# Kernel optimization log

Hardware: AMD Instinct MI355X
Metric: run time of the kernel (lower is better)

Reference implementation:

```python
import jax, jax.numpy as jnp
import numpy as np

# Dimensions
B = 256        # number of graphs
NPG = 128      # nodes per graph (max_nodes; uniform -> to_dense_batch == reshape)
H = 8          # num_heads
DH = 32        # head_dim
HID = H * DH   # hidden_dim = 256
E = 524288     # n_edges
NGT = 20       # num_gate_types
EF = 8         # edge_feat_dim


def setup_inputs() -> dict:
    key = jax.random.key(0)
    ks = jax.random.split(key, 20)
    n_nodes = B * NPG
    x = jax.random.normal(ks[0], (n_nodes, HID), jnp.float32)
    # edges stay within the source node's graph
    src = jax.random.randint(ks[1], (E,), 0, n_nodes, dtype=jnp.int32)
    dst = (src // NPG) * NPG + jax.random.randint(ks[2], (E,), 0, NPG, dtype=jnp.int32)
    edge_index = jnp.stack([src, dst])  # [2, E]
    edge_attr = jax.random.normal(ks[3], (E, EF), jnp.float32)
    edge_gate_type = jax.random.randint(ks[4], (E,), 0, NGT, dtype=jnp.int32)
    batch = (jnp.arange(n_nodes) // NPG).astype(jnp.int32)

    s = 1.0 / np.sqrt(HID)
    def lin(k, din, dout, scale):
        kw, kb = jax.random.split(k)
        return (jax.random.uniform(kw, (din, dout), jnp.float32, -scale, scale),
                jax.random.uniform(kb, (dout,), jnp.float32, -scale, scale))
    Wq, bq = lin(ks[5], HID, HID, s)
    Wk, bk = lin(ks[6], HID, HID, s)
    Wv, bv = lin(ks[7], HID, HID, s)
    Wo, bo = lin(ks[8], HID, HID, s)
    gate_table = jax.random.normal(ks[9], (NGT, H), jnp.float32)
    We, be = lin(ks[10], EF, H, 1.0 / np.sqrt(EF))
    return {"x": x, "edge_attr": edge_attr, "Wq": Wq, "bq": bq, "Wk": Wk, "bk": bk,
            "Wv": Wv, "bv": bv, "Wo": Wo, "bo": bo, "gate_table": gate_table,
            "We": We, "be": be, "edge_index": edge_index,
            "edge_gate_type": edge_gate_type, "batch": batch}


def _edge_bias(edge_index, edge_attr, edge_gate_type, batch, gate_table, We, be):
    src, dst = edge_index[0], edge_index[1]
    eb = batch[src]                       # edge -> graph id
    src_l = src - eb * NPG                # local node index within graph
    dst_l = dst - eb * NPG
    total = gate_table[edge_gate_type] + edge_attr @ We + be   # [E, H]
    bias = jnp.zeros((B, H, NPG, NPG), edge_attr.dtype)
    bias = bias.at[eb, :, src_l, dst_l].add(total)             # forward direction
    rev = jnp.where((src_l != dst_l)[:, None], total, 0.0)     # skip self-loops
    bias = bias.at[eb, :, dst_l, src_l].add(rev)               # reverse direction
    return bias


def reference(x, edge_attr, Wq, bq, Wk, bk, Wv, bv, Wo, bo, gate_table, We, be,
              edge_index, edge_gate_type, batch):
    scale = 1.0 / np.sqrt(DH)
    xd = x.reshape(B, NPG, HID)  # uniform graph sizes -> to_dense_batch is a reshape
    Q = (xd @ Wq + bq).reshape(B, NPG, H, DH).transpose(0, 2, 1, 3)  # [B,H,N,D]
    K = (xd @ Wk + bk).reshape(B, NPG, H, DH).transpose(0, 2, 1, 3)
    V = (xd @ Wv + bv).reshape(B, NPG, H, DH).transpose(0, 2, 1, 3)
    scores = jnp.einsum('bhqd,bhkd->bhqk', Q, K) * scale
    scores = scores + _edge_bias(edge_index, edge_attr, edge_gate_type, batch,
                                 gate_table, We, be)
    attn = jax.nn.softmax(scores, axis=-1)  # node_mask all-True (uniform sizes)
    out = jnp.einsum('bhqk,bhkd->bhqd', attn, V)
    out = out.transpose(0, 2, 1, 3).reshape(B * NPG, HID)
    return out @ Wo + bo
```

## Files before the change

kernel.cpp:

```cpp
#include <hip/hip_runtime.h>
#include <hip/hip_fp16.h>

typedef unsigned short u16;
typedef unsigned int u32;
typedef __attribute__((ext_vector_type(8))) short short8;
typedef __attribute__((ext_vector_type(4))) float f32x4;

#define MFMA16(a, b, c) __builtin_amdgcn_mfma_f32_16x16x32_bf16((a), (b), (c), 0, 0, 0)

#define ESTRIDE 2304

#define FIXSCALE 16777216.0f
#define FIXINV   5.9604644775390625e-8f

__device__ __forceinline__ float b2f(u16 u) {
  union { float f; unsigned int i; } v;
  v.i = ((unsigned int)u) << 16;
  return v.f;
}
__device__ __forceinline__ u16 f2b(float f) {
  union { float f; unsigned int i; } v;
  v.f = f;
  unsigned int x = v.i;
  return (u16)((x + 0x7FFFu + ((x >> 16) & 1u)) >> 16);
}
__device__ __forceinline__ u16 f2h_bits(float f) {
  __half h = __float2half(f);
  u16 b;
  __builtin_memcpy(&b, &h, 2);
  return b;
}
__device__ __forceinline__ float h2f_bits(u16 b) {
  __half h;
  __builtin_memcpy(&h, &b, 2);
  return __half2float(h);
}
__device__ __forceinline__ u32 pk_bf16(float a, float b) {
  return (u32)f2b(a) | ((u32)f2b(b) << 16);
}

__device__ __forceinline__ void gload_lds16(const u16* g, u16* l) {
  __builtin_amdgcn_global_load_lds(
      (const __attribute__((address_space(1))) void*)g,
      (__attribute__((address_space(3))) void*)l, 16, 0, 0);
}

__global__ __launch_bounds__(256) void cvt_wtrans_kernel(
    const float* __restrict__ x, u16* __restrict__ xb,
    const float* __restrict__ W0, const float* __restrict__ W1,
    const float* __restrict__ W2, const float* __restrict__ W3,
    u16* __restrict__ T0, u16* __restrict__ T1,
    u16* __restrict__ T2, u16* __restrict__ T3,
    u32* __restrict__ gfill) {
  int bx = blockIdx.x;
  if (bx < 4096) {
    size_t i = ((size_t)bx * 256 + threadIdx.x) * 8;
    const float4* p = (const float4*)(x + i);
    float4 v0 = p[0], v1 = p[1];
    float vf[8] = {v0.x, v0.y, v0.z, v0.w, v1.x, v1.y, v1.z, v1.w};
    short8 s;
#pragma unroll
    for (int j = 0; j < 8; ++j) s[j] = (short)f2b(vf[j]);
    *(short8*)(xb + i) = s;
  } else if (bx < 4224) {
    int r = bx - 4096;
    const float* W; u16* T;
    switch (r >> 5) {
      case 0: W = W0; T = T0; break;
      case 1: W = W1; T = T1; break;
      case 2: W = W2; T = T2; break;
      default: W = W3; T = T3; break;
    }
    int n = threadIdx.x;
    int k0 = (r & 31) * 8;
    short8 s;
#pragma unroll
    for (int j = 0; j < 8; ++j) s[j] = (short)f2b(W[(size_t)(k0 + j) * 256 + n]);
    *(short8*)(T + (size_t)n * 256 + k0) = s;
  } else {
    int idx = (bx - 4224) * 256 + threadIdx.x;
    gfill[idx] = 0;
  }
}

__global__ __launch_bounds__(256) void edge_build_kernel(
    const int* __restrict__ ei, const float* __restrict__ ea,
    const int* __restrict__ egt, const float* __restrict__ gate_table,
    const float* __restrict__ We, const float* __restrict__ be,
    u32* __restrict__ gfill, u16* __restrict__ etot16,
    u32* __restrict__ epos, int E) {
  __shared__ u32 hist[256];
  __shared__ u32 cursor[256];
  const int tid = threadIdx.x;
  hist[tid] = 0;
  __syncthreads();
  const int base_e = blockIdx.x * 2048;
  int gcache[8];
#pragma unroll
  for (int i = 0; i < 8; ++i) {
    int e = base_e + i * 256 + tid;
    int g = (e < E) ? (ei[e] >> 7) : -1;
    gcache[i] = g;
    if (g >= 0) atomicAdd(&hist[(u32)g], 1u);
  }
  __syncthreads();
  {
    u32 c = hist[tid];
    u32 r = c ? atomicAdd(&gfill[tid * 16], c) : 0u;
    cursor[tid] = (u32)tid * ESTRIDE + r;
  }
  __syncthreads();
#pragma unroll
  for (int i = 0; i < 8; ++i) {
    int g = gcache[i];
    if (g < 0) continue;
    int e = base_e + i * 256 + tid;
    int src = ei[e], dst = ei[E + e];
    int sl = src & 127, dl = dst & 127;
    int gt = egt[e];
    const float4* eap = (const float4*)(ea + (size_t)e * 8);
    float4 e0 = eap[0], e1 = eap[1];
    float eaf[8] = {e0.x, e0.y, e0.z, e0.w, e1.x, e1.y, e1.z, e1.w};
    short8 sv;
#pragma unroll
    for (int h = 0; h < 8; ++h) {
      float s = gate_table[gt * 8 + h] + be[h];
#pragma unroll
      for (int f = 0; f < 8; ++f) s += eaf[f] * We[f * 8 + h];
      sv[h] = (short)f2h_bits(s);
    }
    u32 pos = atomicAdd(&cursor[(u32)g], 1u);
    epos[pos] = (u32)sl | ((u32)dl << 16);
    *(short8*)(etot16 + (size_t)pos * 8) = sv;
  }
}

__global__ __launch_bounds__(256) void etrans_pad_kernel(
    const u16* __restrict__ aos, const u32* __restrict__ gfill,
    u16* __restrict__ soa, u32* __restrict__ epos) {
  int g = blockIdx.y;
  int p = blockIdx.x * 256 + threadIdx.x;
  u32 cnt = gfill[g * 16];
  size_t idx = (size_t)g * ESTRIDE + p;
  const size_t plane = (size_t)256 * ESTRIDE;
  if ((u32)p < cnt) {
    short8 v = *(const short8*)(aos + idx * 8);
#pragma unroll
    for (int h = 0; h < 8; ++h) soa[plane * h + idx] = (u16)v[h];
  } else {
    epos[idx] = 0;
#pragma unroll
    for (int h = 0; h < 8; ++h) soa[plane * h + idx] = 0;
  }
}

template <int NMAT, typename COUT>
__global__ __launch_bounds__(256) void gemm_tiled_kernel(
    const u16* __restrict__ A,
    const u16* __restrict__ T0, const u16* __restrict__ T1,
    const u16* __restrict__ T2,
    const float* __restrict__ b0, const float* __restrict__ b1,
    const float* __restrict__ b2,
    float s0, float s1, float s2,
    COUT* __restrict__ C0, COUT* __restrict__ C1, COUT* __restrict__ C2) {
  __shared__ __align__(16) u16 lA[128 * 64];
  __shared__ __align__(16) u16 lB[128 * 64];

  const int tid = threadIdx.x;
  const int bm = blockIdx.x;
  const int bn = blockIdx.y;
  const int m  = (NMAT == 1) ? 0 : (bn >> 1);
  const int ch = (NMAT == 1) ? bn : (bn & 1);

  const u16* Ts[3] = {T0, T1, T2};
  const float* bs[3] = {b0, b1, b2};
  const float scs[3] = {s0, s1, s2};
  COUT* Cs[3] = {C0, C1, C2};

  const u16* Abase = A + (size_t)(bm * 128) * 256;
  const u16* Bbase = Ts[m] + (size_t)(ch * 128) * 256;

  int srow[4];
  int selem[4];
#pragma unroll
  for (int i = 0; i < 4; ++i) {
    int c = i * 256 + tid;
    int row = c >> 3;
    int q = (c & 7) * 16;
    srow[i] = row;
    selem[i] = (q ^ ((row & 7) << 4)) >> 1;
  }

  const int wid = tid >> 6, lane = tid & 63;
  const int wm = wid >> 1, wn = wid & 1;
  const int quad = lane >> 4, l16 = lane & 15;
  const int swz = (l16 & 7) << 4;

  f32x4 acc[4][4] = {};

#pragma unroll
  for (int kt = 0; kt < 4; ++kt) {
    const int k0 = kt * 64;
    __syncthreads();
#pragma unroll
    for (int i = 0; i < 4; ++i) {
      gload_lds16(Abase + (size_t)srow[i] * 256 + k0 + selem[i],
                  lA + (size_t)(i * 256 + tid) * 8);
      gload_lds16(Bbase + (size_t)srow[i] * 256 + k0 + selem[i],
                  lB + (size_t)(i * 256 + tid) * 8);
    }
    __syncthreads();

#pragma unroll
    for (int ks = 0; ks < 2; ++ks) {
      const int kb = (ks * 64 + quad * 16) ^ swz;
      short8 af[4], bf[4];
#pragma unroll
      for (int i = 0; i < 4; ++i) {
        int arow = wm * 64 + i * 16 + l16;
        af[i] = *(const short8*)((const char*)lA + arow * 128 + kb);
        int brow = wn * 64 + i * 16 + l16;
        bf[i] = *(const short8*)((const char*)lB + brow * 128 + kb);
      }
#pragma unroll
      for (int i = 0; i < 4; ++i)
#pragma unroll
        for (int j = 0; j < 4; ++j)
          acc[i][j] = MFMA16(af[i], bf[j], acc[i][j]);
    }
  }

  const float* bias = bs[m];
  const float sc = scs[m];
  COUT* C = Cs[m];
#pragma unroll
  for (int j = 0; j < 4; ++j) {
    int col = ch * 128 + wn * 64 + j * 16 + l16;
    float bv = bias[col];
#pragma unroll
    for (int i = 0; i < 4; ++i) {
      int row0 = bm * 128 + wm * 64 + i * 16 + quad * 4;
#pragma unroll
      for (int r = 0; r < 4; ++r) {
        float o = (acc[i][j][r] + bv) * sc;
        if constexpr (sizeof(COUT) == 4)
          C[(size_t)(row0 + r) * 256 + col] = o;
        else
          C[(size_t)(row0 + r) * 256 + col] = f2b(o);
      }
    }
  }
}

__global__ __launch_bounds__(512, 4) void attn_kernel(
    const u16* __restrict__ Q, const u16* __restrict__ K,
    const u16* __restrict__ V, const u32* __restrict__ epos,
    const u16* __restrict__ etot16, u16* __restrict__ O) {
  constexpr int LV = 144, LS = 132;
  __shared__ __align__(16) char smem[67584];
  int*   Si  = (int*)smem;
  u32*   Su  = (u32*)smem;
  u16*   Vt  = (u16*)(smem + 34816);
  float* inv = (float*)(smem + 44032);

  const int tid = threadIdx.x;
  const int h = blockIdx.x, b = blockIdx.y;
  const int wid = tid >> 6, lane = tid & 63;
  const int quad = lane >> 4, l16 = lane & 15;

  u32 pd[5]; u16 tb[5];
  {
    const u32* ep = epos + (size_t)b * ESTRIDE + tid;
    const u16* ets = etot16 + (size_t)h * (256 * ESTRIDE) + (size_t)b * ESTRIDE + tid;
#pragma unroll
    for (int i = 0; i < 4; ++i) pd[i] = ep[i * 512];
#pragma unroll
    for (int i = 0; i < 4; ++i) tb[i] = ets[i * 512];
    if (tid < 256) { pd[4] = ep[2048]; tb[4] = ets[2048]; }
  }

  const int vr = tid >> 2, vs = (tid & 3) * 8;
  short8 vreg = *(const short8*)(V + (size_t)(b * 128 + vr) * 256 + h * 32 + vs);

  {
    short8 aq = *(const short8*)(
        Q + (size_t)(b * 128 + wid * 16 + l16) * 256 + h * 32 + quad * 8);
#pragma unroll
    for (int j = 0; j < 8; ++j) {
      short8 bk = *(const short8*)(
          K + (size_t)(b * 128 + j * 16 + l16) * 256 + h * 32 + quad * 8);
      f32x4 z = {0.f, 0.f, 0.f, 0.f};
      f32x4 sv = MFMA16(aq, bk, z);
      const int cswz = (j >> 1) << 3;
#pragma unroll
      for (int r = 0; r < 4; ++r)
        Si[(wid * 16 + quad * 4 + r) * LS + ((j * 16 + l16) ^ cswz)] =
            __float2int_rn(sv[r] * FIXSCALE);
    }
  }
  __syncthreads();

#pragma unroll
  for (int i = 0; i < 5; ++i) {
    if ((i < 4 || tid < 256) && ((pd[i] | (u32)tb[i]) != 0)) {
      int sl = pd[i] & 0xffff, dl = pd[i] >> 16;
      u32 ti = (u32)__float2int_rn(h2f_bits(tb[i]) * FIXSCALE);
      int dls = dl ^ ((dl & 0x60) >> 2);
      int sls = sl ^ ((sl & 0x60) >> 2);
      atomicAdd(&Su[sl * LS + dls], ti);
      if (sl != dl) atomicAdd(&Su[dl * LS + sls], ti);
    }
  }
  __syncthreads();

  u32 pw[16];
  {
    const int row = wid * 16 + l16;
    const int* srow = &Si[row * LS];
    int sv[32];
#pragma unroll
    for (int k = 0; k < 4; ++k) {
      int cbase = 32 * k + 8 * (quad ^ k);
      int4 v0 = *(const int4*)(srow + cbase);
      int4 v1 = *(const int4*)(srow + cbase + 4);
      sv[k * 8 + 0] = v0.x; sv[k * 8 + 1] = v0.y;
      sv[k * 8 + 2] = v0.z; sv[k * 8 + 3] = v0.w;
      sv[k * 8 + 4] = v1.x; sv[k * 8 + 5] = v1.y;
      sv[k * 8 + 6] = v1.z; sv[k * 8 + 7] = v1.w;
    }
    int m = sv[0];
#pragma unroll
    for (int c = 1; c < 32; ++c) m = (sv[c] > m) ? sv[c] : m;
    m = max(m, __shfl_xor(m, 16, 64));
    m = max(m, __shfl_xor(m, 32, 64));
    float sum = 0.f;
#pragma unroll
    for (int w = 0; w < 16; ++w) {
      float p0 = __expf((float)(sv[2 * w + 0] - m) * FIXINV);
      float p1 = __expf((float)(sv[2 * w + 1] - m) * FIXINV);
      sum += p0 + p1;
      pw[w] = pk_bf16(p0, p1);
    }
    sum += __shfl_xor(sum, 16, 64);
    sum += __shfl_xor(sum, 32, 64);
    __syncthreads();
#pragma unroll
    for (int j = 0; j < 8; ++j)
      Vt[(vs + j) * LV + vr] = (u16)vreg[j];
    if (quad == 0) inv[row] = 1.f / sum;
  }
  __syncthreads();

  f32x4 oacc[2] = {};
#pragma unroll
  for (int ks = 0; ks < 4; ++ks) {
    union { u32 w[4]; short8 s; } ap;
#pragma unroll
    for (int j = 0; j < 4; ++j) ap.w[j] = pw[ks * 4 + j];
#pragma unroll
    for (int j = 0; j < 2; ++j) {
      short8 bv = *(short8*)&Vt[(j * 16 + l16) * LV + ks * 32 + quad * 8];
      oacc[j] = MFMA16(ap.s, bv, oacc[j]);
    }
  }
#pragma unroll
  for (int j = 0; j < 2; ++j)
#pragma unroll
    for (int r = 0; r < 4; ++r) {
      int qr = wid * 16 + quad * 4 + r;
      float iv = inv[qr];
      O[(size_t)(b * 128 + qr) * 256 + h * 32 + j * 16 + l16] =
          f2b(oacc[j][r] * iv);
    }
}


extern "C" void kernel_launch(void* const* d_in, const int* in_sizes, int n_in,
                              void* d_out, int out_size, void* d_ws, size_t ws_size,
                              hipStream_t stream) {
  const float* x    = (const float*)d_in[0];
  const float* ea   = (const float*)d_in[1];
  const float* Wq   = (const float*)d_in[2];
  const float* bq   = (const float*)d_in[3];
  const float* Wk   = (const float*)d_in[4];
  const float* bk   = (const float*)d_in[5];
  const float* Wv   = (const float*)d_in[6];
  const float* bv   = (const float*)d_in[7];
  const float* Wo   = (const float*)d_in[8];
  const float* bo   = (const float*)d_in[9];
  const float* gate = (const float*)d_in[10];
  const float* We   = (const float*)d_in[11];
  const float* be   = (const float*)d_in[12];
  const int*   ei   = (const int*)d_in[13];
  const int*   egt  = (const int*)d_in[14];
  const int    E    = in_sizes[14];

  const size_t matBytes = (size_t)32768 * 256 * 2;
  const size_t slots = (size_t)256 * ESTRIDE;

  char* ws = (char*)d_ws;
  u16* Qm = (u16*)ws;
  u16* Km = (u16*)(ws + matBytes);
  u16* Vm = (u16*)(ws + 2 * matBytes);
  u16* Om = (u16*)(ws + 3 * matBytes);
  u16* xb = Om;
  u16*   etA  = (u16*)(ws + 4 * matBytes);
  u16*   etS  = etA + slots * 8;
  u32*   epos = (u32*)(etS + slots * 8);
  u32*   gfill = (u32*)((char*)epos + slots * 4);
  u16*   Wtq = (u16*)((char*)gfill + 4096 * 4);
  u16*   Wtk = Wtq + 65536;
  u16*   Wtv = Wtk + 65536;
  u16*   Wto = Wtv + 65536;

  cvt_wtrans_kernel<<<dim3(4240), dim3(256), 0, stream>>>(
      x, xb, Wq, Wk, Wv, Wo, Wtq, Wtk, Wtv, Wto, gfill);

  edge_build_kernel<<<dim3((E + 2047) / 2048), dim3(256), 0, stream>>>(
      ei, ea, egt, gate, We, be, gfill, etA, epos, E);

  etrans_pad_kernel<<<dim3(ESTRIDE / 256, 256), dim3(256), 0, stream>>>(
      etA, gfill, etS, epos);

  const float qscale = 0.17677669529663687f;
  gemm_tiled_kernel<3, u16><<<dim3(256, 6), dim3(256), 0, stream>>>(
      xb, Wtq, Wtk, Wtv, bq, bk, bv, qscale, 1.f, 1.f, Qm, Km, Vm);

  attn_kernel<<<dim3(8, 256), dim3(512), 0, stream>>>(
      Qm, Km, Vm, epos, etS, Om);

  gemm_tiled_kernel<1, float><<<dim3(256, 2), dim3(256), 0, stream>>>(
      Om, Wto, nullptr, nullptr, bo, nullptr, nullptr, 1.f, 1.f, 1.f,
      (float*)d_out, nullptr, nullptr);
}
```

Before: 220.4 us.

## Write edge bias directly in SoA layout and drop transpose/pad kernel

The edge-build kernel now scatters per-head fp16 edge biases straight into the head-major SoA buffer, so the separate AoS-to-SoA transpose and zero-padding kernel and its extra buffer are removed. Instead of relying on zeroed padding slots, the attention kernel reads the per-graph edge count and skips slots past it. This saves one launch and a full read and write pass over the edge buffer. In exchange, the scattered writes are strided 2-byte stores to eight planes, which may coalesce poorly.

```diff
diff --git a/kernel.cpp b/kernel.cpp
--- a/kernel.cpp
+++ b/kernel.cpp
@@ -87,8 +87,9 @@
     const int* __restrict__ ei, const float* __restrict__ ea,
     const int* __restrict__ egt, const float* __restrict__ gate_table,
     const float* __restrict__ We, const float* __restrict__ be,
-    u32* __restrict__ gfill, u16* __restrict__ etot16,
+    u32* __restrict__ gfill, u16* __restrict__ soa,
     u32* __restrict__ epos, int E) {
+  const size_t plane = (size_t)256 * ESTRIDE;
   __shared__ u32 hist[256];
   __shared__ u32 cursor[256];
   const int tid = threadIdx.x;
@@ -121,36 +122,18 @@
     const float4* eap = (const float4*)(ea + (size_t)e * 8);
     float4 e0 = eap[0], e1 = eap[1];
     float eaf[8] = {e0.x, e0.y, e0.z, e0.w, e1.x, e1.y, e1.z, e1.w};
-    short8 sv;
+    u16 sv[8];
 #pragma unroll
     for (int h = 0; h < 8; ++h) {
       float s = gate_table[gt * 8 + h] + be[h];
 #pragma unroll
       for (int f = 0; f < 8; ++f) s += eaf[f] * We[f * 8 + h];
-      sv[h] = (short)f2h_bits(s);
+      sv[h] = f2h_bits(s);
     }
     u32 pos = atomicAdd(&cursor[(u32)g], 1u);
     epos[pos] = (u32)sl | ((u32)dl << 16);
-    *(short8*)(etot16 + (size_t)pos * 8) = sv;
-  }
-}
-
-__global__ __launch_bounds__(256) void etrans_pad_kernel(
-    const u16* __restrict__ aos, const u32* __restrict__ gfill,
-    u16* __restrict__ soa, u32* __restrict__ epos) {
-  int g = blockIdx.y;
-  int p = blockIdx.x * 256 + threadIdx.x;
-  u32 cnt = gfill[g * 16];
-  size_t idx = (size_t)g * ESTRIDE + p;
-  const size_t plane = (size_t)256 * ESTRIDE;
-  if ((u32)p < cnt) {
-    short8 v = *(const short8*)(aos + idx * 8);
-#pragma unroll
-    for (int h = 0; h < 8; ++h) soa[plane * h + idx] = (u16)v[h];
-  } else {
-    epos[idx] = 0;
-#pragma unroll
-    for (int h = 0; h < 8; ++h) soa[plane * h + idx] = 0;
+#pragma unroll
+    for (int h = 0; h < 8; ++h) soa[plane * h + pos] = sv[h];
   }
 }
 
@@ -255,7 +238,8 @@
 __global__ __launch_bounds__(512, 4) void attn_kernel(
     const u16* __restrict__ Q, const u16* __restrict__ K,
     const u16* __restrict__ V, const u32* __restrict__ epos,
-    const u16* __restrict__ etot16, u16* __restrict__ O) {
+    const u16* __restrict__ etot16, const u32* __restrict__ gfill,
+    u16* __restrict__ O) {
   constexpr int LV = 144, LS = 132;
   __shared__ __align__(16) char smem[67584];
   int*   Si  = (int*)smem;
@@ -268,6 +252,7 @@
   const int wid = tid >> 6, lane = tid & 63;
   const int quad = lane >> 4, l16 = lane & 15;
 
+  const u32 cnt = gfill[b * 16];
   u32 pd[5]; u16 tb[5];
   {
     const u32* ep = epos + (size_t)b * ESTRIDE + tid;
@@ -302,7 +287,9 @@
 
 #pragma unroll
   for (int i = 0; i < 5; ++i) {
-    if ((i < 4 || tid < 256) && ((pd[i] | (u32)tb[i]) != 0)) {
+    u32 slot = (i < 4) ? (u32)(tid + i * 512) : (u32)(2048 + tid);
+    bool live = (i < 4 || tid < 256) && (slot < cnt);
+    if (live) {
       int sl = pd[i] & 0xffff, dl = pd[i] >> 16;
       u32 ti = (u32)__float2int_rn(h2f_bits(tb[i]) * FIXSCALE);
       int dls = dl ^ ((dl & 0x60) >> 2);
@@ -404,8 +391,7 @@
   u16* Vm = (u16*)(ws + 2 * matBytes);
   u16* Om = (u16*)(ws + 3 * matBytes);
   u16* xb = Om;
-  u16*   etA  = (u16*)(ws + 4 * matBytes);
-  u16*   etS  = etA + slots * 8;
+  u16*   etS  = (u16*)(ws + 4 * matBytes);
   u32*   epos = (u32*)(etS + slots * 8);
   u32*   gfill = (u32*)((char*)epos + slots * 4);
   u16*   Wtq = (u16*)((char*)gfill + 4096 * 4);
@@ -417,17 +403,14 @@
       x, xb, Wq, Wk, Wv, Wo, Wtq, Wtk, Wtv, Wto, gfill);
 
   edge_build_kernel<<<dim3((E + 2047) / 2048), dim3(256), 0, stream>>>(
-      ei, ea, egt, gate, We, be, gfill, etA, epos, E);
-
-  etrans_pad_kernel<<<dim3(ESTRIDE / 256, 256), dim3(256), 0, stream>>>(
-      etA, gfill, etS, epos);
+      ei, ea, egt, gate, We, be, gfill, etS, epos, E);
 
   const float qscale = 0.17677669529663687f;
   gemm_tiled_kernel<3, u16><<<dim3(256, 6), dim3(256), 0, stream>>>(
       xb, Wtq, Wtk, Wtv, bq, bk, bv, qscale, 1.f, 1.f, Qm, Km, Vm);
 
   attn_kernel<<<dim3(8, 256), dim3(512), 0, stream>>>(
-      Qm, Km, Vm, epos, etS, Om);
+      Qm, Km, Vm, epos, etS, gfill, Om);
 
   gemm_tiled_kernel<1, float><<<dim3(256, 2), dim3(256), 0, stream>>>(
       Om, Wto, nullptr, nullptr, bo, nullptr, nullptr, 1.f, 1.f, 1.f,
```

After: 242.0 us. +9.8%, slower.
